# Performance work log

Measured on AMD Instinct MI355X. Metric: run time of the kernel, lower is better.

Reference implementation:

```python
import jax, jax.numpy as jnp
import numpy as np

B, S, D, H = 2, 2048, 1024, 16
DEPTH = D // H

def setup_inputs() -> dict:
    key = jax.random.key(0)
    k1, k2, k3 = jax.random.split(key, 3)
    x = jax.random.normal(k1, (B, S, D), dtype=jnp.float32)
    # causal mask (1 = attend, 0 = blocked), broadcastable over batch/heads
    mask = jnp.tril(jnp.ones((S, S), dtype=jnp.int32))[None, None]
    W_qkv = jax.random.normal(k2, (D, 3 * D), dtype=jnp.float32) * (D ** -0.5)
    b_qkv = jnp.zeros((3 * D,), dtype=jnp.float32)
    W_out = jax.random.normal(k3, (D, D), dtype=jnp.float32) * (D ** -0.5)
    b_out = jnp.zeros((D,), dtype=jnp.float32)
    return {"x": x, "mask": mask, "W_qkv": W_qkv, "b_qkv": b_qkv,
            "W_out": W_out, "b_out": b_out}

def reference(x, mask, W_qkv, b_qkv, W_out, b_out):
    b, s, _ = x.shape
    qkv = x @ W_qkv + b_qkv                        # [b, s, 3D]
    qkv = qkv.reshape(b, s, H, 3 * DEPTH)          # matches torch reshape
    qkv = jnp.transpose(qkv, (0, 2, 1, 3))         # [b, h, s, 3*depth]
    q, k, v = jnp.split(qkv, 3, axis=-1)           # each [b, h, s, depth]
    scores = jnp.einsum('bhqd,bhkd->bhqk', q, k) / jnp.sqrt(jnp.float32(DEPTH))
    scores = jnp.where(mask == 0, -jnp.inf, scores)
    attn = jax.nn.softmax(scores, axis=-1)         # dropout: eval mode (identity)
    out = jnp.einsum('bhqk,bhkd->bhqd', attn, v)   # [b, h, s, depth]
    out = jnp.transpose(out, (0, 2, 1, 3)).reshape(b, s, D)
    return out @ W_out + b_out
```

## Files before the change

kernel.cpp:

```cpp
#include <hip/hip_runtime.h>

#define BB 2
#define SS 2048
#define DDIM 1024
#define HH 16
#define DEPTH 64
#define QKVN (3*DDIM)

typedef unsigned short u16;
typedef unsigned int u32;
typedef __attribute__((ext_vector_type(8))) short bf16x8;
typedef __attribute__((ext_vector_type(4))) float f32x4;

__device__ __forceinline__ u16 f2bf(float f){
  union{float f; u32 u;} z; z.f=f;
  u32 r = z.u + 0x7fffu + ((z.u>>16)&1u);
  return (u16)(r>>16);
}
#define NEG_BIG (-1e30f)

typedef const __attribute__((address_space(1))) u32* gas_t;
typedef __attribute__((address_space(3))) u32* las_t;
__device__ __forceinline__ void gl_lds16(const void* g, void* l){
  __builtin_amdgcn_global_load_lds((gas_t)g, (las_t)l, 16, 0, 0);
}

__global__ void convT_k(const float* __restrict__ in, u16* __restrict__ out, int R, int C){
  __shared__ float tile[32][33];
  int c0 = blockIdx.x<<5, r0 = blockIdx.y<<5;
  int tx = threadIdx.x, ty = threadIdx.y;
  for (int i=ty;i<32;i+=8) tile[i][tx] = in[(size_t)(r0+i)*C + c0+tx];
  __syncthreads();
  for (int i=ty;i<32;i+=8) out[(size_t)(c0+i)*R + r0+tx] = f2bf(tile[tx][i]);
}

__global__ void convX_k(const float* __restrict__ in, u16* __restrict__ out){
  size_t i = ((size_t)blockIdx.x*256 + threadIdx.x) * 8;
  float4 a = *(const float4*)(in + i);
  float4 b = *(const float4*)(in + i + 4);
  ushort4 lo = { f2bf(a.x), f2bf(a.y), f2bf(a.z), f2bf(a.w) };
  ushort4 hi = { f2bf(b.x), f2bf(b.y), f2bf(b.z), f2bf(b.w) };
  *(ushort4*)(out + i)     = lo;
  *(ushort4*)(out + i + 4) = hi;
}

__global__ __launch_bounds__(256,2) void gemm_qkv_k(
    const u16* __restrict__ A, const u16* __restrict__ Bt,
    const float* __restrict__ bias,
    u16* __restrict__ Qb, u16* __restrict__ Kb, u16* __restrict__ Vt)
{
  const int K = DDIM;
  __shared__ __align__(16) u16 As[128*32];
  __shared__ __align__(16) u16 Bs[128*32];
  const int tid = threadIdx.x;
  const int m0 = blockIdx.x<<7, n0 = blockIdx.y<<7;
  const int w = tid>>6, lane = tid&63, q = lane>>4, ln = lane&15;
  const int wr = (w>>1)<<6, wc = (w&1)<<6;

  f32x4 acc[4][4];
  #pragma unroll
  for (int i=0;i<4;i++)
    #pragma unroll
    for (int j=0;j<4;j++) acc[i][j] = (f32x4){0.f,0.f,0.f,0.f};

  for (int k0=0;k0<K;k0+=32){
    {
      int c = tid, row = c>>2, off = (c&3)<<3;
      gl_lds16(&A [(size_t)(m0+row)*K + k0 + off], &As[c<<3]);
      gl_lds16(&Bt[(size_t)(n0+row)*K + k0 + off], &Bs[c<<3]);
      c = tid + 256; row = c>>2; off = (c&3)<<3;
      gl_lds16(&A [(size_t)(m0+row)*K + k0 + off], &As[c<<3]);
      gl_lds16(&Bt[(size_t)(n0+row)*K + k0 + off], &Bs[c<<3]);
    }
    __syncthreads();
    bf16x8 af[4], bfr[4];
    #pragma unroll
    for (int i=0;i<4;i++) af[i]  = *(const bf16x8*)&As[((wr + (i<<4) + ln)<<5) + (q<<3)];
    #pragma unroll
    for (int j=0;j<4;j++) bfr[j] = *(const bf16x8*)&Bs[((wc + (j<<4) + ln)<<5) + (q<<3)];
    #pragma unroll
    for (int i=0;i<4;i++)
      #pragma unroll
      for (int j=0;j<4;j++)
        acc[i][j] = __builtin_amdgcn_mfma_f32_16x16x32_bf16(af[i], bfr[j], acc[i][j], 0, 0, 0);
    __syncthreads();
  }

  #pragma unroll
  for (int i=0;i<4;i++){
    const int mmb = m0 + wr + (i<<4) + (q<<2);
    const int bsel = mmb >> 11;
    const int sb   = mmb & 2047;
    #pragma unroll
    for (int j=0;j<4;j++){
      const int n = n0 + wc + (j<<4) + ln;
      const int h = n / 192;
      const int rr = n - h*192;
      const int bh = (bsel<<4) + h;
      const float bv = bias[n];
      if (rr < 64){
        u16* dst = Qb + (size_t)bh*SS*DEPTH + rr;
        #pragma unroll
        for (int r=0;r<4;r++) dst[(size_t)(sb+r)*DEPTH] = f2bf((acc[i][j][r] + bv)*0.125f);
      } else if (rr < 128){
        u16* dst = Kb + (size_t)bh*SS*DEPTH + (rr-64);
        #pragma unroll
        for (int r=0;r<4;r++) dst[(size_t)(sb+r)*DEPTH] = f2bf(acc[i][j][r] + bv);
      } else {
        ushort4 pv = { f2bf(acc[i][j][0] + bv), f2bf(acc[i][j][1] + bv),
                       f2bf(acc[i][j][2] + bv), f2bf(acc[i][j][3] + bv) };
        *(ushort4*)(Vt + ((size_t)bh*DEPTH + (rr-128))*SS + sb) = pv;
      }
    }
  }
}

__global__ __launch_bounds__(256,4) void attn_k(
    u16* __restrict__ Qb, const u16* __restrict__ Kb, const u16* __restrict__ Vt)
{
  __shared__ __align__(16) u16 Ks[64*64];
  __shared__ __align__(16) u16 VsT[64*64];
  __shared__ __align__(16) u16 ps[4][16*72];

  const int tid = threadIdx.x, w = tid>>6, lane = tid&63, q = lane>>4, ln = lane&15;
  const int bh = blockIdx.x;
  const int y  = blockIdx.y, sgrp = y>>3, rr_ = y&7;
  const int qt = (sgrp==0) ? 31-rr_ : (sgrp==1) ? 16+rr_ : (sgrp==2) ? 15-rr_ : rr_;
  const int r0 = qt<<6;
  const size_t kbase = (size_t)bh*SS*DEPTH;
  const size_t vbase = (size_t)bh*DEPTH*SS;

  bf16x8 qf[2];
  #pragma unroll
  for (int ks=0;ks<2;ks++)
    qf[ks] = *(const bf16x8*)(Qb + kbase + (size_t)(r0 + (w<<4) + ln)*DEPTH + (ks<<5) + (q<<3));

  f32x4 o[4];
  #pragma unroll
  for (int nt=0;nt<4;nt++) o[nt] = (f32x4){0.f,0.f,0.f,0.f};
  float m_r[4], l_r[4];
  #pragma unroll
  for (int r=0;r<4;r++){ m_r[r] = NEG_BIG; l_r[r] = 0.f; }

  const int T = qt + 1;
  for (int t=0;t<T;t++){
    __syncthreads();
    #pragma unroll
    for (int p=0;p<2;p++){
      const int e = (p*256 + tid)*8;
      gl_lds16(Kb + kbase + (size_t)(t<<6)*DEPTH + e, &Ks[e]);
      const int j = e>>6, d = e&63;
      gl_lds16(Vt + vbase + (size_t)j*SS + (t<<6) + d, &VsT[e]);
    }
    __syncthreads();

    f32x4 sc[4];
    #pragma unroll
    for (int jt=0;jt<4;jt++) sc[jt] = (f32x4){0.f,0.f,0.f,0.f};
    #pragma unroll
    for (int ks=0;ks<2;ks++){
      #pragma unroll
      for (int jt=0;jt<4;jt++){
        bf16x8 kf = *(const bf16x8*)&Ks[(((jt<<4)+ln)<<6) + (ks<<5) + (q<<3)];
        sc[jt] = __builtin_amdgcn_mfma_f32_16x16x32_bf16(qf[ks], kf, sc[jt], 0, 0, 0);
      }
    }

    if (t == T-1){
      const int rowb = r0 + (w<<4) + (q<<2);
      #pragma unroll
      for (int jt=0;jt<4;jt++){
        const int col = (t<<6) + (jt<<4) + ln;
        #pragma unroll
        for (int r=0;r<4;r++)
          if (col > rowb + r) sc[jt][r] = NEG_BIG;
      }
    }

    float alpha_r[4];
    #pragma unroll
    for (int r=0;r<4;r++){
      float mt = fmaxf(fmaxf(sc[0][r], sc[1][r]), fmaxf(sc[2][r], sc[3][r]));
      #pragma unroll
      for (int off=1; off<16; off<<=1) mt = fmaxf(mt, __shfl_xor(mt, off));
      const float mnew = fmaxf(m_r[r], mt);
      alpha_r[r] = __expf(m_r[r] - mnew);
      float p0 = __expf(sc[0][r]-mnew), p1 = __expf(sc[1][r]-mnew);
      float p2 = __expf(sc[2][r]-mnew), p3 = __expf(sc[3][r]-mnew);
      const int mrow = (q<<2) + r;
      ps[w][mrow*72 +      ln] = f2bf(p0);
      ps[w][mrow*72 + 16 + ln] = f2bf(p1);
      ps[w][mrow*72 + 32 + ln] = f2bf(p2);
      ps[w][mrow*72 + 48 + ln] = f2bf(p3);
      float psum = (p0+p1)+(p2+p3);
      #pragma unroll
      for (int off=1; off<16; off<<=1) psum += __shfl_xor(psum, off);
      l_r[r] = l_r[r]*alpha_r[r] + psum;
      m_r[r] = mnew;
    }
    #pragma unroll
    for (int nt=0;nt<4;nt++)
      #pragma unroll
      for (int r=0;r<4;r++) o[nt][r] *= alpha_r[r];

    __syncthreads();

    #pragma unroll
    for (int ks=0;ks<2;ks++){
      bf16x8 pa = *(const bf16x8*)&ps[w][ln*72 + (ks<<5) + (q<<3)];
      #pragma unroll
      for (int nt=0;nt<4;nt++){
        bf16x8 vf = *(const bf16x8*)&VsT[(((nt<<4)+ln)<<6) + (ks<<5) + (q<<3)];
        o[nt] = __builtin_amdgcn_mfma_f32_16x16x32_bf16(pa, vf, o[nt], 0, 0, 0);
      }
    }
  }

  #pragma unroll
  for (int r=0;r<4;r++){
    const float rl = 1.f / fmaxf(l_r[r], 1e-30f);
    const int s = r0 + (w<<4) + (q<<2) + r;
    #pragma unroll
    for (int nt=0;nt<4;nt++)
      Qb[kbase + (size_t)s*DEPTH + (nt<<4) + ln] = f2bf(o[nt][r] * rl);
  }
}

__global__ __launch_bounds__(256,2) void gemm_out_k(
    const u16* __restrict__ Aq, const u16* __restrict__ Bt,
    const float* __restrict__ bias, float* __restrict__ out)
{
  const int K = DDIM;
  __shared__ __align__(16) u16 As[128*32];
  __shared__ __align__(16) u16 Bs[128*32];
  const int tid = threadIdx.x;
  const int m0 = blockIdx.x<<7, n0 = blockIdx.y<<7;
  const int bsel = m0>>11, ms = m0&2047;
  const int w = tid>>6, lane = tid&63, q = lane>>4, ln = lane&15;
  const int wr = (w>>1)<<6, wc = (w&1)<<6;

  f32x4 acc[4][4];
  #pragma unroll
  for (int i=0;i<4;i++)
    #pragma unroll
    for (int j=0;j<4;j++) acc[i][j] = (f32x4){0.f,0.f,0.f,0.f};

  for (int k0=0;k0<K;k0+=32){
    const size_t abase = (size_t)((bsel<<4) + (k0>>6))*SS*DEPTH + (k0&63);
    {
      int c = tid, row = c>>2, off = (c&3)<<3;
      gl_lds16(&Aq[abase + (size_t)(ms+row)*DEPTH + off], &As[c<<3]);
      gl_lds16(&Bt[(size_t)(n0+row)*K + k0 + off],        &Bs[c<<3]);
      c = tid + 256; row = c>>2; off = (c&3)<<3;
      gl_lds16(&Aq[abase + (size_t)(ms+row)*DEPTH + off], &As[c<<3]);
      gl_lds16(&Bt[(size_t)(n0+row)*K + k0 + off],        &Bs[c<<3]);
    }
    __syncthreads();
    bf16x8 af[4], bfr[4];
    #pragma unroll
    for (int i=0;i<4;i++) af[i]  = *(const bf16x8*)&As[((wr + (i<<4) + ln)<<5) + (q<<3)];
    #pragma unroll
    for (int j=0;j<4;j++) bfr[j] = *(const bf16x8*)&Bs[((wc + (j<<4) + ln)<<5) + (q<<3)];
    #pragma unroll
    for (int i=0;i<4;i++)
      #pragma unroll
      for (int j=0;j<4;j++)
        acc[i][j] = __builtin_amdgcn_mfma_f32_16x16x32_bf16(af[i], bfr[j], acc[i][j], 0, 0, 0);
    __syncthreads();
  }

  #pragma unroll
  for (int i=0;i<4;i++){
    #pragma unroll
    for (int j=0;j<4;j++){
      const int n = n0 + wc + (j<<4) + ln;
      const float bv = bias[n];
      #pragma unroll
      for (int r=0;r<4;r++){
        const int mm = m0 + wr + (i<<4) + (q<<2) + r;
        out[(size_t)mm*DDIM + n] = acc[i][j][r] + bv;
      }
    }
  }
}

extern "C" void kernel_launch(void* const* d_in, const int* in_sizes, int n_in,
                              void* d_out, int out_size, void* d_ws, size_t ws_size,
                              hipStream_t stream)
{
  int ix = 0, iw = 2, ibq = 3, iwo = 4, ibo = 5;
  if (n_in == 5){ iw = 1; ibq = 2; iwo = 3; ibo = 4; }
  const float* x  = (const float*)d_in[ix];
  const float* Wq = (const float*)d_in[iw];
  const float* bq = (const float*)d_in[ibq];
  const float* Wo = (const float*)d_in[iwo];
  const float* bo = (const float*)d_in[ibo];
  float* out = (float*)d_out;

  u16* ws  = (u16*)d_ws;
  u16* Wqt = ws;
  u16* Wot = Wqt + (size_t)QKVN*DDIM;
  u16* Qb  = Wot + (size_t)DDIM*DDIM;
  u16* Kb  = Qb  + (size_t)BB*HH*SS*DEPTH;
  u16* Vt  = Kb  + (size_t)BB*HH*SS*DEPTH;
  u16* xb  = Vt  + (size_t)BB*HH*SS*DEPTH;

  convT_k<<<dim3(QKVN/32, DDIM/32), dim3(32,8), 0, stream>>>(Wq, Wqt, DDIM, QKVN);
  convT_k<<<dim3(DDIM/32, DDIM/32), dim3(32,8), 0, stream>>>(Wo, Wot, DDIM, DDIM);
  convX_k<<<dim3(BB*SS*DDIM/2048), 256, 0, stream>>>(x, xb);

  gemm_qkv_k<<<dim3(BB*SS/128, QKVN/128), 256, 0, stream>>>(xb, Wqt, bq, Qb, Kb, Vt);
  attn_k    <<<dim3(BB*HH, 32),           256, 0, stream>>>(Qb, Kb, Vt);
  gemm_out_k<<<dim3(BB*SS/128, DDIM/128), 256, 0, stream>>>(Qb, Wot, bo, out);
}
```

Baseline: 241.6 us.

## Enlarge attention query tile to 128 rows with padded LDS tiles

```diff
diff --git a/kernel.cpp b/kernel.cpp
--- a/kernel.cpp
+++ b/kernel.cpp
@@ -115,114 +115,132 @@
   }
 }
 
-__global__ __launch_bounds__(256,4) void attn_k(
+__global__ __launch_bounds__(256,2) void attn_k(
     u16* __restrict__ Qb, const u16* __restrict__ Kb, const u16* __restrict__ Vt)
 {
-  __shared__ __align__(16) u16 Ks[64*64];
-  __shared__ __align__(16) u16 VsT[64*64];
-  __shared__ __align__(16) u16 ps[4][16*72];
+  __shared__ __align__(16) u16 Ks[64*72];
+  __shared__ __align__(16) u16 VsT[64*72];
+  __shared__ __align__(16) u16 ps[4][32*72];
 
   const int tid = threadIdx.x, w = tid>>6, lane = tid&63, q = lane>>4, ln = lane&15;
   const int bh = blockIdx.x;
-  const int y  = blockIdx.y, sgrp = y>>3, rr_ = y&7;
-  const int qt = (sgrp==0) ? 31-rr_ : (sgrp==1) ? 16+rr_ : (sgrp==2) ? 15-rr_ : rr_;
-  const int r0 = qt<<6;
+  const int y  = blockIdx.y;
+  const int qt = (y<8) ? (15-y) : (y-8);
+  const int r0 = qt<<7;
   const size_t kbase = (size_t)bh*SS*DEPTH;
   const size_t vbase = (size_t)bh*DEPTH*SS;
 
-  bf16x8 qf[2];
-  #pragma unroll
-  for (int ks=0;ks<2;ks++)
-    qf[ks] = *(const bf16x8*)(Qb + kbase + (size_t)(r0 + (w<<4) + ln)*DEPTH + (ks<<5) + (q<<3));
-
-  f32x4 o[4];
-  #pragma unroll
-  for (int nt=0;nt<4;nt++) o[nt] = (f32x4){0.f,0.f,0.f,0.f};
-  float m_r[4], l_r[4];
-  #pragma unroll
-  for (int r=0;r<4;r++){ m_r[r] = NEG_BIG; l_r[r] = 0.f; }
-
-  const int T = qt + 1;
+  bf16x8 qf[2][2];
+  #pragma unroll
+  for (int rg=0;rg<2;rg++)
+    #pragma unroll
+    for (int ks=0;ks<2;ks++)
+      qf[rg][ks] = *(const bf16x8*)(Qb + kbase +
+          (size_t)(r0 + (w<<5) + (rg<<4) + ln)*DEPTH + (ks<<5) + (q<<3));
+
+  f32x4 o[2][4];
+  float m_r[2][4], l_r[2][4];
+  #pragma unroll
+  for (int rg=0;rg<2;rg++){
+    #pragma unroll
+    for (int nt=0;nt<4;nt++) o[rg][nt] = (f32x4){0.f,0.f,0.f,0.f};
+    #pragma unroll
+    for (int r=0;r<4;r++){ m_r[rg][r] = NEG_BIG; l_r[rg][r] = 0.f; }
+  }
+
+  const int T = (qt<<1) + 2;
   for (int t=0;t<T;t++){
     __syncthreads();
     #pragma unroll
     for (int p=0;p<2;p++){
       const int e = (p*256 + tid)*8;
-      gl_lds16(Kb + kbase + (size_t)(t<<6)*DEPTH + e, &Ks[e]);
       const int j = e>>6, d = e&63;
-      gl_lds16(Vt + vbase + (size_t)j*SS + (t<<6) + d, &VsT[e]);
-    }
-    __syncthreads();
-
-    f32x4 sc[4];
-    #pragma unroll
-    for (int jt=0;jt<4;jt++) sc[jt] = (f32x4){0.f,0.f,0.f,0.f};
-    #pragma unroll
-    for (int ks=0;ks<2;ks++){
-      #pragma unroll
-      for (int jt=0;jt<4;jt++){
-        bf16x8 kf = *(const bf16x8*)&Ks[(((jt<<4)+ln)<<6) + (ks<<5) + (q<<3)];
-        sc[jt] = __builtin_amdgcn_mfma_f32_16x16x32_bf16(qf[ks], kf, sc[jt], 0, 0, 0);
-      }
-    }
-
-    if (t == T-1){
-      const int rowb = r0 + (w<<4) + (q<<2);
-      #pragma unroll
-      for (int jt=0;jt<4;jt++){
-        const int col = (t<<6) + (jt<<4) + ln;
-        #pragma unroll
-        for (int r=0;r<4;r++)
-          if (col > rowb + r) sc[jt][r] = NEG_BIG;
-      }
-    }
-
-    float alpha_r[4];
+      *(uint4*)&Ks[j*72 + d]  = *(const uint4*)(Kb + kbase + (size_t)(t<<6)*DEPTH + e);
+      *(uint4*)&VsT[j*72 + d] = *(const uint4*)(Vt + vbase + (size_t)j*SS + (t<<6) + d);
+    }
+    __syncthreads();
+
+    #pragma unroll
+    for (int rg=0;rg<2;rg++){
+      f32x4 sc[4];
+      #pragma unroll
+      for (int jt=0;jt<4;jt++) sc[jt] = (f32x4){0.f,0.f,0.f,0.f};
+      #pragma unroll
+      for (int ks=0;ks<2;ks++){
+        #pragma unroll
+        for (int jt=0;jt<4;jt++){
+          bf16x8 kf = *(const bf16x8*)&Ks[((jt<<4)+ln)*72 + (ks<<5) + (q<<3)];
+          sc[jt] = __builtin_amdgcn_mfma_f32_16x16x32_bf16(qf[rg][ks], kf, sc[jt], 0, 0, 0);
+        }
+      }
+
+      if (t >= (qt<<1)){
+        const int rowb = r0 + (w<<5) + (rg<<4) + (q<<2);
+        #pragma unroll
+        for (int jt=0;jt<4;jt++){
+          const int col = (t<<6) + (jt<<4) + ln;
+          #pragma unroll
+          for (int r=0;r<4;r++)
+            if (col > rowb + r) sc[jt][r] = NEG_BIG;
+        }
+      }
+
+      float alpha_r[4];
+      #pragma unroll
+      for (int r=0;r<4;r++){
+        float mt = fmaxf(fmaxf(sc[0][r], sc[1][r]), fmaxf(sc[2][r], sc[3][r]));
+        #pragma unroll
+        for (int off=1; off<16; off<<=1) mt = fmaxf(mt, __shfl_xor(mt, off));
+        const float mnew = fmaxf(m_r[rg][r], mt);
+        alpha_r[r] = __expf(m_r[rg][r] - mnew);
+        const int mrow = (rg<<4) + (q<<2) + r;
+        float psum = 0.f;
+        #pragma unroll
+        for (int jt=0;jt<4;jt++){
+          const float p = __expf(sc[jt][r] - mnew);
+          psum += p;
+          const u32 myv = (u32)f2bf(p);
+          const u32 ov  = __shfl_xor(myv, 1);
+          if ((ln & 1) == 0)
+            *(u32*)&ps[w][mrow*72 + (jt<<4) + ln] = myv | (ov<<16);
+        }
+        #pragma unroll
+        for (int off=1; off<16; off<<=1) psum += __shfl_xor(psum, off);
+        l_r[rg][r] = l_r[rg][r]*alpha_r[r] + psum;
+        m_r[rg][r] = mnew;
+      }
+      #pragma unroll
+      for (int nt=0;nt<4;nt++)
+        #pragma unroll
+        for (int r=0;r<4;r++) o[rg][nt][r] *= alpha_r[r];
+    }
+
+    __syncthreads();
+
+    #pragma unroll
+    for (int rg=0;rg<2;rg++){
+      #pragma unroll
+      for (int ks=0;ks<2;ks++){
+        bf16x8 pa = *(const bf16x8*)&ps[w][((rg<<4)+ln)*72 + (ks<<5) + (q<<3)];
+        #pragma unroll
+        for (int nt=0;nt<4;nt++){
+          bf16x8 vf = *(const bf16x8*)&VsT[((nt<<4)+ln)*72 + (ks<<5) + (q<<3)];
+          o[rg][nt] = __builtin_amdgcn_mfma_f32_16x16x32_bf16(pa, vf, o[rg][nt], 0, 0, 0);
+        }
+      }
+    }
+  }
+
+  #pragma unroll
+  for (int rg=0;rg<2;rg++){
     #pragma unroll
     for (int r=0;r<4;r++){
-      float mt = fmaxf(fmaxf(sc[0][r], sc[1][r]), fmaxf(sc[2][r], sc[3][r]));
-      #pragma unroll
-      for (int off=1; off<16; off<<=1) mt = fmaxf(mt, __shfl_xor(mt, off));
-      const float mnew = fmaxf(m_r[r], mt);
-      alpha_r[r] = __expf(m_r[r] - mnew);
-      float p0 = __expf(sc[0][r]-mnew), p1 = __expf(sc[1][r]-mnew);
-      float p2 = __expf(sc[2][r]-mnew), p3 = __expf(sc[3][r]-mnew);
-      const int mrow = (q<<2) + r;
-      ps[w][mrow*72 +      ln] = f2bf(p0);
-      ps[w][mrow*72 + 16 + ln] = f2bf(p1);
-      ps[w][mrow*72 + 32 + ln] = f2bf(p2);
-      ps[w][mrow*72 + 48 + ln] = f2bf(p3);
-      float psum = (p0+p1)+(p2+p3);
-      #pragma unroll
-      for (int off=1; off<16; off<<=1) psum += __shfl_xor(psum, off);
-      l_r[r] = l_r[r]*alpha_r[r] + psum;
-      m_r[r] = mnew;
-    }
-    #pragma unroll
-    for (int nt=0;nt<4;nt++)
-      #pragma unroll
-      for (int r=0;r<4;r++) o[nt][r] *= alpha_r[r];
-
-    __syncthreads();
-
-    #pragma unroll
-    for (int ks=0;ks<2;ks++){
-      bf16x8 pa = *(const bf16x8*)&ps[w][ln*72 + (ks<<5) + (q<<3)];
-      #pragma unroll
-      for (int nt=0;nt<4;nt++){
-        bf16x8 vf = *(const bf16x8*)&VsT[(((nt<<4)+ln)<<6) + (ks<<5) + (q<<3)];
-        o[nt] = __builtin_amdgcn_mfma_f32_16x16x32_bf16(pa, vf, o[nt], 0, 0, 0);
-      }
-    }
-  }
-
-  #pragma unroll
-  for (int r=0;r<4;r++){
-    const float rl = 1.f / fmaxf(l_r[r], 1e-30f);
-    const int s = r0 + (w<<4) + (q<<2) + r;
-    #pragma unroll
-    for (int nt=0;nt<4;nt++)
-      Qb[kbase + (size_t)s*DEPTH + (nt<<4) + ln] = f2bf(o[nt][r] * rl);
+      const float rl = 1.f / fmaxf(l_r[rg][r], 1e-30f);
+      const int s = r0 + (w<<5) + (rg<<4) + (q<<2) + r;
+      #pragma unroll
+      for (int nt=0;nt<4;nt++)
+        Qb[kbase + (size_t)s*DEPTH + (nt<<4) + ln] = f2bf(o[rg][nt][r] * rl);
+    }
   }
 }
 
@@ -310,6 +328,6 @@
   convX_k<<<dim3(BB*SS*DDIM/2048), 256, 0, stream>>>(x, xb);
 
   gemm_qkv_k<<<dim3(BB*SS/128, QKVN/128), 256, 0, stream>>>(xb, Wqt, bq, Qb, Kb, Vt);
-  attn_k    <<<dim3(BB*HH, 32),           256, 0, stream>>>(Qb, Kb, Vt);
+  attn_k    <<<dim3(BB*HH, 16),           256, 0, stream>>>(Qb, Kb, Vt);
   gemm_out_k<<<dim3(BB*SS/128, DDIM/128), 256, 0, stream>>>(Qb, Wot, bo, out);
 }
```

Result: slower. 295.4 us (+22.2%).
